# Kernel tuning notes

Measured on AMD Instinct MI355X. Metric: run time of the kernel, lower is better.

## Reference

```python
import jax, jax.numpy as jnp
import numpy as np

BN_EPS = 1e-5

def setup_inputs() -> dict:
    key = jax.random.key(0)
    ks = jax.random.split(key, 8)
    N, E, D = 50000, 800000, 128
    x = jax.random.normal(ks[0], (N, D), dtype=jnp.float32)
    edge_index = jax.random.randint(ks[1], (2, E), 0, N, dtype=jnp.int64)
    s = 1.0 / np.sqrt(D)
    W1 = jax.random.uniform(ks[2], (D, D), jnp.float32, -s, s)
    b1 = jax.random.uniform(ks[3], (D,), jnp.float32, -s, s)
    W2 = jax.random.uniform(ks[4], (D, D), jnp.float32, -s, s)
    b2 = jax.random.uniform(ks[5], (D,), jnp.float32, -s, s)
    g1 = jnp.ones((D,), jnp.float32); be1 = jnp.zeros((D,), jnp.float32)
    g2 = jnp.ones((D,), jnp.float32); be2 = jnp.zeros((D,), jnp.float32)
    eps = jnp.zeros((), jnp.float32)  # learnable GIN epsilon (train_eps=True)
    return {"x": x, "edge_index": edge_index, "eps": eps,
            "W1": W1, "b1": b1, "g1": g1, "be1": be1,
            "W2": W2, "b2": b2, "g2": g2, "be2": be2}

def _batchnorm(h, gamma, beta):
    # training-mode BatchNorm1d over node axis (biased variance)
    mu = jnp.mean(h, axis=0)
    var = jnp.mean(jnp.square(h - mu), axis=0)
    return (h - mu) * jax.lax.rsqrt(var + BN_EPS) * gamma + beta

def reference(x, edge_index, eps, W1, b1, g1, be1, W2, b2, g2, be2):
    N = x.shape[0]
    src, dst = edge_index[0], edge_index[1]
    # GIN aggregation: sum of neighbor features (scatter-add to target nodes)
    agg = jax.ops.segment_sum(x[src], dst, num_segments=N)  # [N, D]
    h = (1.0 + eps) * x + agg
    # MLP: Linear -> BN -> ReLU -> Linear
    h = h @ W1.T + b1
    h = jax.nn.relu(_batchnorm(h, g1, be1))
    h = h @ W2.T + b2
    # outer BatchNorm + ReLU
    return jax.nn.relu(_batchnorm(h, g2, be2))
```

## Files before the change

### kernel.cpp

```cpp
#include <hip/hip_runtime.h>
#include <hip/hip_bf16.h>


#define DIM 128
#define SUB 2
#define CAP 32
#define KMAX 64

typedef unsigned short u16;
typedef __attribute__((ext_vector_type(8))) short short8;
typedef __attribute__((ext_vector_type(8))) unsigned short ushort8;
typedef __attribute__((ext_vector_type(4))) float f32x4;

__device__ inline u16 f2b(float f) {
  unsigned int u = __builtin_bit_cast(unsigned int, f);
  u += 0x7fffu + ((u >> 16) & 1u);
  return (u16)(u >> 16);
}
__device__ inline float b2f(u16 b) {
  unsigned int u = ((unsigned int)b) << 16;
  return __builtin_bit_cast(float, u);
}

__global__ __launch_bounds__(256) void prep_kernel(
    const float* __restrict__ W1, const float* __restrict__ W2,
    const float* __restrict__ x, int* __restrict__ cursor,
    u16* __restrict__ wb1, u16* __restrict__ wb2, u16* __restrict__ xb,
    int Z, int NX) {
  int i = blockIdx.x * blockDim.x + threadIdx.x;
  const int stride = gridDim.x * blockDim.x;
  const int e1 = Z + 4096, e2 = Z + 8192, e3 = Z + 8192 + NX;
  for (; i < e3; i += stride) {
    if (i < Z) {
      int4 z = {0, 0, 0, 0};
      reinterpret_cast<int4*>(cursor)[i] = z;
    } else if (i < e1) {
      const int j = i - Z;
      const float4 v = reinterpret_cast<const float4*>(W1)[j];
      ushort4 o = {f2b(v.x), f2b(v.y), f2b(v.z), f2b(v.w)};
      reinterpret_cast<ushort4*>(wb1)[j] = o;
    } else if (i < e2) {
      const int j = i - e1;
      const float4 v = reinterpret_cast<const float4*>(W2)[j];
      ushort4 o = {f2b(v.x), f2b(v.y), f2b(v.z), f2b(v.w)};
      reinterpret_cast<ushort4*>(wb2)[j] = o;
    } else {
      const int j = i - e2;
      const float4 v = reinterpret_cast<const float4*>(x)[j];
      ushort4 o = {f2b(v.x), f2b(v.y), f2b(v.z), f2b(v.w)};
      reinterpret_cast<ushort4*>(xb)[j] = o;
    }
  }
}

__global__ __launch_bounds__(256) void reorder_kernel(
    const int* __restrict__ ei, int* __restrict__ cursor,
    u16* __restrict__ buckets, int E, int T) {
  const int t = blockIdx.x * blockDim.x + threadIdx.x;
  const int way = t & 1;
  int s[8], d[8], p[8];
  bool valid[8];
#pragma unroll
  for (int i = 0; i < 8; ++i) {
    const int e = t + i * T;
    valid[i] = e < E;
    const int ec = valid[i] ? e : 0;
    s[i] = ei[ec];
    d[i] = ei[E + ec];
  }
#pragma unroll
  for (int i = 0; i < 8; ++i)
    p[i] = valid[i] ? atomicAdd(&cursor[d[i] * SUB + way], 1) : CAP;
#pragma unroll
  for (int i = 0; i < 8; ++i)
    if (p[i] < CAP) buckets[d[i] * KMAX + way * CAP + p[i]] = (u16)s[i];
}

__global__ __launch_bounds__(256) void aggregate_kernel(
    const u16* __restrict__ xb, const int* __restrict__ cursor,
    const u16* __restrict__ buckets, const float* __restrict__ epsp,
    u16* __restrict__ hb, int N) {
  const int wid = threadIdx.x >> 6;
  const int lane = threadIdx.x & 63;
  const int node = blockIdx.x * 4 + wid;
  if (node >= N) return;
  const int slot = lane >> 4;
  const int chunk = lane & 15;
  int c0 = cursor[node * SUB + 0]; if (c0 > CAP) c0 = CAP;
  int c1 = cursor[node * SUB + 1]; if (c1 > CAP) c1 = CAP;
  const int deg = c0 + c1;
  const u16* bk = buckets + node * KMAX;

  int my = 0;
  if (lane < c0) my = bk[lane];
  else if (lane - c0 < c1) my = bk[CAP + lane - c0];

  float acc[8];
#pragma unroll
  for (int f = 0; f < 8; ++f) acc[f] = 0.f;

  for (int t0 = 0; t0 < deg; t0 += 4) {
    const int idx = t0 + slot;
    const int src = __shfl(my, idx);
    const ushort8 v = *reinterpret_cast<const ushort8*>(xb + (size_t)src * DIM + chunk * 8);
    if (idx < deg) {
#pragma unroll
      for (int f = 0; f < 8; ++f) acc[f] += b2f(v[f]);
    }
  }
#pragma unroll
  for (int f = 0; f < 8; ++f) {
    acc[f] += __shfl_xor(acc[f], 16);
    acc[f] += __shfl_xor(acc[f], 32);
  }
  if (slot == 0) {
    const float k = 1.0f + epsp[0];
    const ushort8 xv = *reinterpret_cast<const ushort8*>(xb + (size_t)node * DIM + chunk * 8);
    ushort8 o;
#pragma unroll
    for (int f = 0; f < 8; ++f) o[f] = f2b(acc[f] + k * b2f(xv[f]));
    *reinterpret_cast<ushort8*>(hb + (size_t)node * DIM + chunk * 8) = o;
  }
}

template <int FUSE>
__global__ __launch_bounds__(256) void gemm_mfma_kernel(
    const void* __restrict__ Av, const u16* __restrict__ Wb,
    const float* __restrict__ bias, const float* __restrict__ statsIn,
    const float* __restrict__ gamma, const float* __restrict__ beta,
    void* __restrict__ Cv, float* __restrict__ statsOut, int N, float Ninv) {
  __shared__ float sred[4][DIM];
  __shared__ float qred[4][DIM];
  __shared__ float ssc[DIM];
  __shared__ float ssh[DIM];
  if (FUSE) {
    const int t = threadIdx.x;
    if (t < DIM) {
      const float mu = statsIn[t] * Ninv;
      const float var = statsIn[DIM + t] * Ninv - mu * mu;
      const float sc = gamma[t] * rsqrtf(var + 1e-5f);
      ssc[t] = sc;
      ssh[t] = beta[t] - mu * sc;
    }
    __syncthreads();
  }
  const int lane = threadIdx.x & 63;
  const int wid = threadIdx.x >> 6;
  const int l15 = lane & 15;
  const int lg = lane >> 4;
  const int wrow = blockIdx.x * 64 + wid * 16;

  f32x4 acc[8];
#pragma unroll
  for (int ni = 0; ni < 8; ++ni) acc[ni] = (f32x4){0.f, 0.f, 0.f, 0.f};

  int arow = wrow + l15;
  if (arow >= N) arow = N - 1;

#pragma unroll
  for (int kb = 0; kb < 4; ++kb) {
    const int k0 = kb * 32 + lg * 8;
    short8 a;
    if (FUSE) {
      const float* A = (const float*)Av + (size_t)arow * DIM + k0;
      const float4 v0 = *reinterpret_cast<const float4*>(A);
      const float4 v1 = *reinterpret_cast<const float4*>(A + 4);
      a[0] = (short)f2b(fmaxf(fmaf(v0.x, ssc[k0 + 0], ssh[k0 + 0]), 0.f));
      a[1] = (short)f2b(fmaxf(fmaf(v0.y, ssc[k0 + 1], ssh[k0 + 1]), 0.f));
      a[2] = (short)f2b(fmaxf(fmaf(v0.z, ssc[k0 + 2], ssh[k0 + 2]), 0.f));
      a[3] = (short)f2b(fmaxf(fmaf(v0.w, ssc[k0 + 3], ssh[k0 + 3]), 0.f));
      a[4] = (short)f2b(fmaxf(fmaf(v1.x, ssc[k0 + 4], ssh[k0 + 4]), 0.f));
      a[5] = (short)f2b(fmaxf(fmaf(v1.y, ssc[k0 + 5], ssh[k0 + 5]), 0.f));
      a[6] = (short)f2b(fmaxf(fmaf(v1.z, ssc[k0 + 6], ssh[k0 + 6]), 0.f));
      a[7] = (short)f2b(fmaxf(fmaf(v1.w, ssc[k0 + 7], ssh[k0 + 7]), 0.f));
    } else {
      a = *reinterpret_cast<const short8*>((const u16*)Av + (size_t)arow * DIM + k0);
    }
#pragma unroll
    for (int ni = 0; ni < 8; ++ni) {
      const short8 b = *reinterpret_cast<const short8*>(Wb + (ni * 16 + l15) * DIM + k0);
      acc[ni] = __builtin_amdgcn_mfma_f32_16x16x32_bf16(a, b, acc[ni], 0, 0, 0);
    }
  }

  const int rbase = wrow + lg * 4;
#pragma unroll
  for (int ni = 0; ni < 8; ++ni) {
    const int col = ni * 16 + l15;
    const float bv = bias[col];
    float s = 0.f, q = 0.f;
#pragma unroll
    for (int r = 0; r < 4; ++r) {
      const int row = rbase + r;
      if (row < N) {
        const float v = acc[ni][r] + bv;
        if (FUSE) {
          const u16 bb = f2b(v);
          const float vr = b2f(bb);
          ((u16*)Cv)[(size_t)row * DIM + col] = bb;
          s += vr;
          q = fmaf(vr, vr, q);
        } else {
          ((float*)Cv)[(size_t)row * DIM + col] = v;
          s += v;
          q = fmaf(v, v, q);
        }
      }
    }
    s += __shfl_xor(s, 16); s += __shfl_xor(s, 32);
    q += __shfl_xor(q, 16); q += __shfl_xor(q, 32);
    if (lg == 0) { sred[wid][col] = s; qred[wid][col] = q; }
  }
  __syncthreads();
  const int t = threadIdx.x;
  if (t < DIM) {
    unsafeAtomicAdd(&statsOut[t], sred[0][t] + sred[1][t] + sred[2][t] + sred[3][t]);
  } else {
    const int c = t - DIM;
    unsafeAtomicAdd(&statsOut[DIM + c], qred[0][c] + qred[1][c] + qred[2][c] + qred[3][c]);
  }
}

__global__ __launch_bounds__(256) void bnrelu_kernel(
    const u16* __restrict__ hb, float* __restrict__ out,
    const float* __restrict__ stats, const float* __restrict__ gamma,
    const float* __restrict__ beta, float Ninv, int total8) {
  __shared__ float ssc[DIM];
  __shared__ float ssh[DIM];
  {
    const int t = threadIdx.x;
    if (t < DIM) {
      const float mu = stats[t] * Ninv;
      const float var = stats[DIM + t] * Ninv - mu * mu;
      const float sc = gamma[t] * rsqrtf(var + 1e-5f);
      ssc[t] = sc;
      ssh[t] = beta[t] - mu * sc;
    }
    __syncthreads();
  }
  int i = blockIdx.x * blockDim.x + threadIdx.x;
  const int stride = gridDim.x * blockDim.x;
  for (; i < total8; i += stride) {
    const int c0 = (i * 8) & (DIM - 1);
    const ushort8 v = reinterpret_cast<const ushort8*>(hb)[i];
    float4 o0, o1;
    o0.x = fmaxf(fmaf(b2f(v[0]), ssc[c0 + 0], ssh[c0 + 0]), 0.f);
    o0.y = fmaxf(fmaf(b2f(v[1]), ssc[c0 + 1], ssh[c0 + 1]), 0.f);
    o0.z = fmaxf(fmaf(b2f(v[2]), ssc[c0 + 2], ssh[c0 + 2]), 0.f);
    o0.w = fmaxf(fmaf(b2f(v[3]), ssc[c0 + 3], ssh[c0 + 3]), 0.f);
    o1.x = fmaxf(fmaf(b2f(v[4]), ssc[c0 + 4], ssh[c0 + 4]), 0.f);
    o1.y = fmaxf(fmaf(b2f(v[5]), ssc[c0 + 5], ssh[c0 + 5]), 0.f);
    o1.z = fmaxf(fmaf(b2f(v[6]), ssc[c0 + 6], ssh[c0 + 6]), 0.f);
    o1.w = fmaxf(fmaf(b2f(v[7]), ssc[c0 + 7], ssh[c0 + 7]), 0.f);
    reinterpret_cast<float4*>(out)[i * 2] = o0;
    reinterpret_cast<float4*>(out)[i * 2 + 1] = o1;
  }
}

extern "C" void kernel_launch(void* const* d_in, const int* in_sizes, int n_in,
                              void* d_out, int out_size, void* d_ws, size_t ws_size,
                              hipStream_t stream) {
  const float* x   = (const float*)d_in[0];
  const int*   ei  = (const int*)d_in[1];
  const float* eps = (const float*)d_in[2];
  const float* W1  = (const float*)d_in[3];
  const float* b1  = (const float*)d_in[4];
  const float* g1  = (const float*)d_in[5];
  const float* be1 = (const float*)d_in[6];
  const float* W2  = (const float*)d_in[7];
  const float* b2  = (const float*)d_in[8];
  const float* g2  = (const float*)d_in[9];
  const float* be2 = (const float*)d_in[10];
  float* out = (float*)d_out;

  const int N = in_sizes[0] / DIM;
  const int E = in_sizes[1] / 2;

  u16* hb      = (u16*)d_ws;
  u16* wb1     = hb + (size_t)N * DIM;
  u16* wb2     = wb1 + DIM * DIM;
  u16* buckets = wb2 + DIM * DIM;
  int* cursor  = (int*)(buckets + (size_t)N * KMAX);
  float* stats1 = (float*)(cursor + SUB * N);
  float* stats2 = stats1 + 256;

  u16* xb = (u16*)d_out;

  const int Z  = (SUB * N + 512 + 3) / 4;
  const int NX = N * DIM / 4;
  const float Ninv = 1.0f / N;

  prep_kernel<<<2048, 256, 0, stream>>>(W1, W2, x, cursor, wb1, wb2, xb, Z, NX);

  const int nth = (E + 7) / 8;
  const int rblocks = (nth + 255) / 256;
  reorder_kernel<<<rblocks, 256, 0, stream>>>(ei, cursor, buckets, E, rblocks * 256);

  aggregate_kernel<<<(N + 3) / 4, 256, 0, stream>>>(xb, cursor, buckets, eps, hb, N);

  const int gblocks = (N + 63) / 64;
  gemm_mfma_kernel<0><<<gblocks, 256, 0, stream>>>(
      hb, wb1, b1, nullptr, nullptr, nullptr, (float*)d_out, stats1, N, Ninv);
  gemm_mfma_kernel<1><<<gblocks, 256, 0, stream>>>(
      (float*)d_out, wb2, b2, stats1, g1, be1, hb, stats2, N, Ninv);
  bnrelu_kernel<<<2048, 256, 0, stream>>>(hb, out, stats2, g2, be2, Ninv, N * (DIM / 8));
}
```

Baseline: 260.4 us.

## Fuse prep and edge reorder into one kernel with partitioned destination ranges

Merges the bf16 conversion kernel and the edge-bucketing kernel into a single launch. Each block does both a slice of the conversion work and a pass over an edge slice, alternating the order between groups of blocks so memory-bound conversion overlaps atomic-heavy bucketing. Edges are filtered into 8 destination partitions, one per block in a group, to localise the atomics and bucket writes. Cursor zeroing moves to a hipMemsetAsync. In exchange, every edge's destination index is now read by 8 blocks, raising index read traffic, and the bucket fill order changes.

```diff
diff --git a/kernel.cpp b/kernel.cpp
--- a/kernel.cpp
+++ b/kernel.cpp
@@ -6,6 +6,7 @@
 #define SUB 2
 #define CAP 32
 #define KMAX 64
+#define RBLK 2048
 
 typedef unsigned short u16;
 typedef __attribute__((ext_vector_type(8))) short short8;
@@ -22,58 +23,55 @@
   return __builtin_bit_cast(float, u);
 }
 
-__global__ __launch_bounds__(256) void prep_kernel(
+__global__ __launch_bounds__(256) void prep_reorder_kernel(
     const float* __restrict__ W1, const float* __restrict__ W2,
-    const float* __restrict__ x, int* __restrict__ cursor,
+    const float* __restrict__ x, const int* __restrict__ ei,
+    int* __restrict__ cursor, u16* __restrict__ buckets,
     u16* __restrict__ wb1, u16* __restrict__ wb2, u16* __restrict__ xb,
-    int Z, int NX) {
-  int i = blockIdx.x * blockDim.x + threadIdx.x;
-  const int stride = gridDim.x * blockDim.x;
-  const int e1 = Z + 4096, e2 = Z + 8192, e3 = Z + 8192 + NX;
-  for (; i < e3; i += stride) {
-    if (i < Z) {
-      int4 z = {0, 0, 0, 0};
-      reinterpret_cast<int4*>(cursor)[i] = z;
-    } else if (i < e1) {
-      const int j = i - Z;
-      const float4 v = reinterpret_cast<const float4*>(W1)[j];
-      ushort4 o = {f2b(v.x), f2b(v.y), f2b(v.z), f2b(v.w)};
-      reinterpret_cast<ushort4*>(wb1)[j] = o;
-    } else if (i < e2) {
-      const int j = i - e1;
-      const float4 v = reinterpret_cast<const float4*>(W2)[j];
-      ushort4 o = {f2b(v.x), f2b(v.y), f2b(v.z), f2b(v.w)};
-      reinterpret_cast<ushort4*>(wb2)[j] = o;
+    int E, float p8N, int CT, int perC) {
+  const int bid = blockIdx.x;
+  const int phase = (bid >> 3) & 1;
+
+#pragma unroll
+  for (int ph = 0; ph < 2; ++ph) {
+    if ((ph ^ phase) == 0) {
+      const int beg = bid * perC;
+      const int end = min(CT, beg + perC);
+      for (int i = beg + (int)threadIdx.x; i < end; i += 256) {
+        if (i < 4096) {
+          const float4 v = reinterpret_cast<const float4*>(W1)[i];
+          ushort4 o = {f2b(v.x), f2b(v.y), f2b(v.z), f2b(v.w)};
+          reinterpret_cast<ushort4*>(wb1)[i] = o;
+        } else if (i < 8192) {
+          const int j = i - 4096;
+          const float4 v = reinterpret_cast<const float4*>(W2)[j];
+          ushort4 o = {f2b(v.x), f2b(v.y), f2b(v.z), f2b(v.w)};
+          reinterpret_cast<ushort4*>(wb2)[j] = o;
+        } else {
+          const int j = i - 8192;
+          const float4 v = reinterpret_cast<const float4*>(x)[j];
+          ushort4 o = {f2b(v.x), f2b(v.y), f2b(v.z), f2b(v.w)};
+          reinterpret_cast<ushort4*>(xb)[j] = o;
+        }
+      }
     } else {
-      const int j = i - e2;
-      const float4 v = reinterpret_cast<const float4*>(x)[j];
-      ushort4 o = {f2b(v.x), f2b(v.y), f2b(v.z), f2b(v.w)};
-      reinterpret_cast<ushort4*>(xb)[j] = o;
-    }
-  }
-}
-
-__global__ __launch_bounds__(256) void reorder_kernel(
-    const int* __restrict__ ei, int* __restrict__ cursor,
-    u16* __restrict__ buckets, int E, int T) {
-  const int t = blockIdx.x * blockDim.x + threadIdx.x;
-  const int way = t & 1;
-  int s[8], d[8], p[8];
-  bool valid[8];
-#pragma unroll
-  for (int i = 0; i < 8; ++i) {
-    const int e = t + i * T;
-    valid[i] = e < E;
-    const int ec = valid[i] ? e : 0;
-    s[i] = ei[ec];
-    d[i] = ei[E + ec];
-  }
-#pragma unroll
-  for (int i = 0; i < 8; ++i)
-    p[i] = valid[i] ? atomicAdd(&cursor[d[i] * SUB + way], 1) : CAP;
-#pragma unroll
-  for (int i = 0; i < 8; ++i)
-    if (p[i] < CAP) buckets[d[i] * KMAX + way * CAP + p[i]] = (u16)s[i];
+      const int part = bid & 7;
+      const int slice = bid >> 3;
+      const int perE = (E + 255) >> 8;
+      const int beg = slice * perE;
+      const int end = min(E, beg + perE);
+      const int way = threadIdx.x & 1;
+      for (int e = beg + (int)threadIdx.x; e < end; e += 256) {
+        const int d = ei[E + e];
+        int p = (int)((float)d * p8N);
+        if (p > 7) p = 7;
+        if (p != part) continue;
+        const int s = ei[e];
+        const int pos = atomicAdd(&cursor[d * SUB + way], 1);
+        if (pos < CAP) buckets[d * KMAX + way * CAP + pos] = (u16)s;
+      }
+    }
+  }
 }
 
 __global__ __launch_bounds__(256) void aggregate_kernel(
@@ -286,15 +284,16 @@
 
   u16* xb = (u16*)d_out;
 
-  const int Z  = (SUB * N + 512 + 3) / 4;
   const int NX = N * DIM / 4;
+  const int CT = 8192 + NX;
+  const int perC = (CT + RBLK - 1) / RBLK;
   const float Ninv = 1.0f / N;
-
-  prep_kernel<<<2048, 256, 0, stream>>>(W1, W2, x, cursor, wb1, wb2, xb, Z, NX);
-
-  const int nth = (E + 7) / 8;
-  const int rblocks = (nth + 255) / 256;
-  reorder_kernel<<<rblocks, 256, 0, stream>>>(ei, cursor, buckets, E, rblocks * 256);
+  const float p8N = 8.0f / N;
+
+  hipMemsetAsync(cursor, 0, (size_t)(SUB * N + 512) * sizeof(int), stream);
+
+  prep_reorder_kernel<<<RBLK, 256, 0, stream>>>(
+      W1, W2, x, ei, cursor, buckets, wb1, wb2, xb, E, p8N, CT, perC);
 
   aggregate_kernel<<<(N + 3) / 4, 256, 0, stream>>>(xb, cursor, buckets, eps, hb, N);
 
```

Result: faster. 253.8 us (-2.5%).
